# Kernel optimization log

Measured on AMD Instinct MI355X. Metric: run time of the kernel, lower is better.

The kernel has to match this reference:

```python
import jax, jax.numpy as jnp
import numpy as np

B, C = 8, 2048          # batch, out_dim (projection channels)
HG = WG = 32            # global crop feature map
HL = WL = 12            # local crop feature map
STUDENT_TEMP = 0.1
TEMP_SCHEDULE = np.concatenate([np.linspace(0.04, 0.07, 30), np.ones(100 - 30) * 0.07])

# Fixed relative boxes (x1, x2, y1, y2) per (iq, v) crop pair, shared across the
# batch so grid shapes are static. Source computes grid_H from teacher_feat.shape[0]
# (= C, a quirk of the original code) and grid_W from shape[1] (= spatial H); boxes
# are chosen so resulting grids are ~[22-25, 22-24].
PAIRS = [
    (0, 1, (-0.80, 0.70, -0.500, -0.475), (-0.90, 0.60, -0.60, 0.60)),
    (0, 2, (-0.75, 0.75,  0.100,  0.125), (-0.80, 0.80, -0.80, 0.80)),
    (0, 3, (-0.60, 0.90, -0.200, -0.178), (-0.70, 0.90, -0.90, 0.70)),
    (1, 0, (-0.70, 0.80,  0.300,  0.322), (-0.85, 0.65, -0.50, 0.90)),
    (1, 2, (-0.90, 0.50, -0.100, -0.076), (-0.60, 0.95, -0.95, 0.60)),
    (1, 3, (-0.50, 0.95,  0.200,  0.224), (-0.90, 0.90, -0.40, 0.95)),
]


def _grid_dims(box, Hc, Wc):
    x1, x2, y1, y2 = box
    return int(abs(y1 - y2) / 2 * Hc), int(abs(x1 - x2) / 2 * Wc)  # (grid_H, grid_W)


def _make_grid(box, gH, gW):
    # Faithful to source: meshgrid([linspace(y1,y2,gH), linspace(x1,x2,gW)]),
    # stacked so channel 0 holds the y-linspace (which grid_sample reads as x).
    x1, x2, y1, y2 = box
    yy, xx = jnp.meshgrid(jnp.linspace(y1, y2, gH), jnp.linspace(x1, x2, gW), indexing='ij')
    return jnp.stack([yy, xx], axis=-1)  # [gH, gW, 2]


def _grid_sample_border(img, grid):
    # torch.nn.functional.grid_sample, bilinear, padding_mode='border',
    # align_corners=False. img: [B, C, H, W], grid: [gH, gW, 2] (same grid per batch).
    H, W = img.shape[-2], img.shape[-1]
    gx, gy = grid[..., 0], grid[..., 1]
    ix = jnp.clip((gx + 1.0) * (W * 0.5) - 0.5, 0.0, W - 1.0)  # border: clip coords
    iy = jnp.clip((gy + 1.0) * (H * 0.5) - 0.5, 0.0, H - 1.0)
    x0f, y0f = jnp.floor(ix), jnp.floor(iy)
    wx = (ix - x0f)[None, None]  # [1,1,gH,gW]
    wy = (iy - y0f)[None, None]
    x0 = x0f.astype(jnp.int32)
    y0 = y0f.astype(jnp.int32)
    x1 = jnp.minimum(x0 + 1, W - 1)
    y1 = jnp.minimum(y0 + 1, H - 1)
    v00 = img[:, :, y0, x0]
    v01 = img[:, :, y0, x1]
    v10 = img[:, :, y1, x0]
    v11 = img[:, :, y1, x1]
    return (1.0 - wy) * ((1.0 - wx) * v00 + wx * v01) + wy * ((1.0 - wx) * v10 + wx * v11)


def setup_inputs() -> dict:
    key = jax.random.key(0)
    ks = jax.random.split(key, 7)
    return {
        'student_g0': jax.random.normal(ks[0], (B, C, HG, WG), jnp.float32),
        'student_g1': jax.random.normal(ks[1], (B, C, HG, WG), jnp.float32),
        'student_l0': jax.random.normal(ks[2], (B, C, HL, WL), jnp.float32),
        'student_l1': jax.random.normal(ks[3], (B, C, HL, WL), jnp.float32),
        'teacher_g0': jax.random.normal(ks[4], (B, C, HG, WG), jnp.float32),
        'teacher_g1': jax.random.normal(ks[5], (B, C, HG, WG), jnp.float32),
        'center': jax.random.normal(ks[6], (1, C), jnp.float32) * 0.1,
        'epoch': 5,
    }


def reference(student_g0, student_g1, student_l0, student_l1,
              teacher_g0, teacher_g1, center, epoch):
    temp = float(TEMP_SCHEDULE[epoch])
    students = [s / STUDENT_TEMP for s in (student_g0, student_g1, student_l0, student_l1)]
    cen = center[:, :, None, None]  # [1,C,1,1]
    cteach = [jax.nn.softmax((t - cen) / temp, axis=1) for t in (teacher_g0, teacher_g1)]

    losses = []
    for iq, v, tbox, sbox in PAIRS:
        tfeat = cteach[iq]   # [B,C,H,W]
        sfeat = students[v]  # [B,C,h,w]
        # Faithful: source passes (shape[0]=C, shape[1]=spatial H) as (H, W).
        gH, gW = _grid_dims(tbox, C, tfeat.shape[2])
        t_common = jax.lax.stop_gradient(_grid_sample_border(tfeat, _make_grid(tbox, gH, gW)))
        s_common = _grid_sample_border(sfeat, _make_grid(sbox, gH, gW))
        # cross-entropy over channels -> [B, gH, gW]
        loss = (-t_common * jax.nn.log_softmax(s_common, axis=1)).sum(axis=1)
        losses.append(loss.reshape(-1))
    return jnp.concatenate(losses).mean()
```

## Files before the change

### kernel.cpp

```cpp
#include <hip/hip_runtime.h>
#include <hip/hip_fp16.h>

#define NPOS 26688

struct PairInfo {
  int iq, v, Hs, gH, gW, base, per;
  unsigned magicPer, magicW;
  int tOfs, tN, tCb;
  int sN, sCb;
  float tx1, tx2, ty1, ty2;
  float sx1, sx2, sy1, sy2;
};

__constant__ PairInfo g_pairs[6] = {
  {0,1,32,25,24,    0,600, 7158279u,178956971u,    0,2, 7, 22,5, -0.80f,0.70f,-0.500f,-0.475f,  -0.90f,0.60f,-0.60f,0.60f},
  {0,2,12,25,24, 4800,600, 7158279u,178956971u,  512,2,17, 12,0, -0.75f,0.75f, 0.100f, 0.125f,  -0.80f,0.80f,-0.80f,0.80f},
  {0,3,12,22,24, 9600,528, 8134408u,178956971u, 1024,2,12, 12,0, -0.60f,0.90f,-0.200f,-0.178f,  -0.70f,0.90f,-0.90f,0.70f},
  {1,0,32,22,24,13824,528, 8134408u,178956971u, 1536,2,20, 24,7, -0.70f,0.80f, 0.300f, 0.322f,  -0.85f,0.65f,-0.50f,0.90f},
  {1,2,12,24,22,18048,528, 8134408u,195225787u, 2048,3,13, 12,0, -0.90f,0.50f,-0.100f,-0.076f,  -0.60f,0.95f,-0.95f,0.60f},
  {1,3,12,24,23,22272,552, 7780739u,186737709u, 2816,3,18, 12,0, -0.50f,0.95f, 0.200f, 0.224f,  -0.90f,0.90f,-0.40f,0.95f},
};

__constant__ int g_tentX[2][8] = {
  { 7, 8,12,13,17,18,-100,-100},
  {13,14,15,18,19,20,  20,  21},
};
__constant__ int g_tentO[2][8] = {
  {   0,   0,1024,1024, 512, 512,   0,   0},
  {2048,2048,2048,2816,2816,2816,1536,1536},
};
__constant__ int g_tentN[2][8] = {
  {2,2,2,2,2,2,2,2},
  {3,3,3,3,3,3,2,2},
};
__constant__ int g_tentC[2][8] = {
  {0,1,0,1,0,1,0,0},
  {0,1,2,0,1,2,0,1},
};
__constant__ int g_cumTex[6] = {0, 512, 1024, 1536, 2048, 2816};
__constant__ int g_tN[6]    = {2, 2, 2, 2, 3, 3};
__constant__ int g_tCb[6]   = {7, 17, 12, 20, 13, 18};

__device__ inline float get_invtemp(const int* __restrict__ ep) {
  int e = ep[0];
  e = e < 0 ? 0 : (e > 99 ? 99 : e);
  float temp = (e < 30) ? (0.04f + (float)e * (0.03f / 29.0f)) : 0.07f;
  return 1.0f / temp;
}

__device__ inline float sel4(const float4& v, int q) {
  return q == 0 ? v.x : q == 1 ? v.y : q == 2 ? v.z : v.w;
}

typedef _Float16 hv2 __attribute__((ext_vector_type(2)));
__device__ inline float fdot2f(__half2 a, __half2 b, float c) {
#if defined(__has_builtin)
#if __has_builtin(__builtin_amdgcn_fdot2)
  return __builtin_amdgcn_fdot2(*reinterpret_cast<hv2*>(&a),
                                *reinterpret_cast<hv2*>(&b), c, false);
#else
  float2 af = __half22float2(a), bf = __half22float2(b);
  return fmaf(af.x, bf.x, fmaf(af.y, bf.y, c));
#endif
#else
  float2 af = __half22float2(a), bf = __half22float2(b);
  return fmaf(af.x, bf.x, fmaf(af.y, bf.y, c));
#endif
}

__global__ __launch_bounds__(256) void dino_phase1(
    const float* __restrict__ tg0, const float* __restrict__ tg1,
    const float* __restrict__ cen, const int* __restrict__ ep,
    float* __restrict__ part_m, float* __restrict__ part_s,
    __half* __restrict__ Tc,
    const float* __restrict__ sl0, const float* __restrict__ sl1,
    __half* __restrict__ Sl0, __half* __restrict__ Sl1,
    const float* __restrict__ sg0, const float* __restrict__ sg1,
    __half* __restrict__ Sg0, __half* __restrict__ Sg1) {
  __shared__ float smem[2960];
  int bid = blockIdx.x;
  int t = threadIdx.x;

  if (bid < 4096) {
    int chunk = bid & 7;
    int y = (bid >> 3) & 31;
    int b = (bid >> 8) & 7;
    int view = bid >> 11;
    const float* __restrict__ src = view ? tg1 : tg0;
    float invtemp = get_invtemp(ep);

    float* cenl = smem;
    float* pm   = smem + 256;
    float* ps   = smem + 1312;
    float* pm2  = smem + 2368;
    float* ps2  = smem + 2632;
    float* cm   = smem + 2896;

    cenl[t] = cen[chunk * 256 + t];
    __syncthreads();

    int xg = t & 7, sub = t >> 3;
    const float* sp = src + (((size_t)(b * 2048 + chunk * 256 + sub)) * 32 + y) * 32 + xg * 4;
    float4 lg[8];
#pragma unroll
    for (int k = 0; k < 8; ++k) {
      float4 v = *reinterpret_cast<const float4*>(sp + (size_t)k * 32768);
      float cv = cenl[k * 32 + sub];
      lg[k].x = (v.x - cv) * invtemp;
      lg[k].y = (v.y - cv) * invtemp;
      lg[k].z = (v.z - cv) * invtemp;
      lg[k].w = (v.w - cv) * invtemp;
    }
    float4 mx = lg[0];
#pragma unroll
    for (int k = 1; k < 8; ++k) {
      mx.x = fmaxf(mx.x, lg[k].x); mx.y = fmaxf(mx.y, lg[k].y);
      mx.z = fmaxf(mx.z, lg[k].z); mx.w = fmaxf(mx.w, lg[k].w);
    }
    float4 s = make_float4(0.f, 0.f, 0.f, 0.f);
#pragma unroll
    for (int k = 0; k < 8; ++k) {
      s.x += __expf(lg[k].x - mx.x); s.y += __expf(lg[k].y - mx.y);
      s.z += __expf(lg[k].z - mx.z); s.w += __expf(lg[k].w - mx.w);
    }
    pm[sub * 33 + xg * 4 + 0] = mx.x; ps[sub * 33 + xg * 4 + 0] = s.x;
    pm[sub * 33 + xg * 4 + 1] = mx.y; ps[sub * 33 + xg * 4 + 1] = s.y;
    pm[sub * 33 + xg * 4 + 2] = mx.z; ps[sub * 33 + xg * 4 + 2] = s.z;
    pm[sub * 33 + xg * 4 + 3] = mx.w; ps[sub * 33 + xg * 4 + 3] = s.w;
    __syncthreads();
    {
      int x = t & 31, g = t >> 5;
      float m0 = pm[(g * 4 + 0) * 33 + x], m1 = pm[(g * 4 + 1) * 33 + x];
      float m2 = pm[(g * 4 + 2) * 33 + x], m3 = pm[(g * 4 + 3) * 33 + x];
      float M = fmaxf(fmaxf(m0, m1), fmaxf(m2, m3));
      float S = ps[(g * 4 + 0) * 33 + x] * __expf(m0 - M)
              + ps[(g * 4 + 1) * 33 + x] * __expf(m1 - M)
              + ps[(g * 4 + 2) * 33 + x] * __expf(m2 - M)
              + ps[(g * 4 + 3) * 33 + x] * __expf(m3 - M);
      pm2[g * 33 + x] = M; ps2[g * 33 + x] = S;
    }
    __syncthreads();
    if (t < 32) {
      float M = pm2[t];
#pragma unroll
      for (int g = 1; g < 8; ++g) M = fmaxf(M, pm2[g * 33 + t]);
      float S = 0.f;
#pragma unroll
      for (int g = 0; g < 8; ++g) S += ps2[g * 33 + t] * __expf(pm2[g * 33 + t] - M);
      part_m[bid * 32 + t] = M;
      part_s[bid * 32 + t] = S;
      cm[t] = M;
    }
    __syncthreads();
    int nent = view ? 8 : 6;
#pragma unroll
    for (int e = 0; e < 8; ++e) {
      if (e < nent) {
        int ex = g_tentX[view][e];
        if ((ex >> 2) == xg) {
          int q = ex & 3;
          float cmx = cm[ex & 31];
          int tex = g_tentO[view][e] + (b * 32 + y) * g_tentN[view][e] + g_tentC[view][e];
          tex = min(max(tex, 0), 3583);
          size_t base = (size_t)tex * 2048 + chunk * 256 + sub;
#pragma unroll
          for (int k = 0; k < 8; ++k)
            Tc[base + k * 32] = __float2half(sel4(lg[k], q) - cmx);
        }
      }
    }
    return;
  }

  if (bid < 6144) {
    float* tile = smem;
    int lb = bid - 4096;
    int ct = lb & 127;
    int g = lb >> 7;
    int b = g & 7;
    int vv = g >> 3;
    const float* __restrict__ src = vv ? sl1 : sl0;
    __half* __restrict__ dst = vv ? Sl1 : Sl0;
    const float* sp = src + ((size_t)(b * 2048 + ct * 16)) * 144;
#pragma unroll
    for (int k = 0; k < 9; ++k) {
      int idx = t + 256 * k;
      int c = idx / 144;
      int yx = idx - c * 144;
      tile[c * 145 + yx] = sp[idx] * 10.f;
    }
    __syncthreads();
    __half* dp = dst + ((size_t)(b * 144)) * 2048 + ct * 16;
#pragma unroll
    for (int k = 0; k < 2; ++k) {
      int u = t + 256 * k;
      if (u < 288) {
        int yx = u >> 1, q8 = (u & 1) * 8;
        __half hv[8];
#pragma unroll
        for (int j = 0; j < 8; ++j) hv[j] = __float2half(tile[(q8 + j) * 145 + yx]);
        *reinterpret_cast<float4*>(dp + (size_t)yx * 2048 + q8) =
            *reinterpret_cast<float4*>(hv);
      }
    }
    return;
  }

  float* tile = smem;
  int lb = bid - 6144;
  int ct = lb & 31;
  int t2 = lb >> 5;
  int yi = t2 % 26;
  int g = t2 / 26;
  int y = yi + 1;
  int b = g & 7;
  int which = g >> 3;
  const float* __restrict__ src = which ? sg1 : sg0;
  __half* __restrict__ dst = which ? Sg1 : Sg0;
  int cb = which ? 5 : 7;
  int n = which ? 22 : 24;

  int xg = t & 7, ch = t >> 3;
  const float* sp = src + (((size_t)(b * 2048 + ct * 64 + ch)) * 32 + y) * 32 + xg * 4;
  float4 v0 = *reinterpret_cast<const float4*>(sp);
  float4 v1 = *reinterpret_cast<const float4*>(sp + 32768);
  tile[ch * 33 + xg * 4 + 0] = v0.x * 10.f;
  tile[ch * 33 + xg * 4 + 1] = v0.y * 10.f;
  tile[ch * 33 + xg * 4 + 2] = v0.z * 10.f;
  tile[ch * 33 + xg * 4 + 3] = v0.w * 10.f;
  tile[(ch + 32) * 33 + xg * 4 + 0] = v1.x * 10.f;
  tile[(ch + 32) * 33 + xg * 4 + 1] = v1.y * 10.f;
  tile[(ch + 32) * 33 + xg * 4 + 2] = v1.z * 10.f;
  tile[(ch + 32) * 33 + xg * 4 + 3] = v1.w * 10.f;
  __syncthreads();
  int xx = t >> 3, ccq = (t & 7) * 8;
  if (xx >= cb && xx < cb + n) {
    __half hv[8];
#pragma unroll
    for (int j = 0; j < 8; ++j) hv[j] = __float2half(tile[(ccq + j) * 33 + xx]);
    __half* dp = dst + ((size_t)((b * 32 + y) * n + (xx - cb))) * 2048 + ct * 64 + ccq;
    *reinterpret_cast<float4*>(dp) = *reinterpret_cast<float4*>(hv);
  }
}

union H8 { uint4 u; __half2 h[4]; };

__global__ __launch_bounds__(256) void dino_probs(
    const __half* __restrict__ Tc, __half* __restrict__ Tp,
    const float* __restrict__ part_m, const float* __restrict__ part_s) {
  __shared__ float pm8[8], ps8[8];
  int bid = blockIdx.x;
  int t = threadIdx.x;
  int p = 0;
#pragma unroll
  for (int q = 1; q < 6; ++q) p += (bid >= g_cumTex[q]) ? 1 : 0;
  int r = bid - g_cumTex[p];
  int n = g_tN[p];
  int by = (n == 2) ? (r >> 1) : (r / 3);
  by = min(max(by, 0), 255);
  int ci = min(max(r - by * n, 0), n - 1);
  int x = g_tCb[p] + ci;
  int view = (p >= 3) ? 1 : 0;
  int b = by >> 5, y = by & 31;
  int texRow = ((view * 8 + b) * 32 + y);
  if (t < 8) {
    pm8[t] = part_m[(texRow * 8 + t) * 32 + x];
    ps8[t] = part_s[(texRow * 8 + t) * 32 + x];
  }
  __syncthreads();
  float M = pm8[0];
#pragma unroll
  for (int c = 1; c < 8; ++c) M = fmaxf(M, pm8[c]);
  float S = 0.f;
#pragma unroll
  for (int c = 0; c < 8; ++c) S += ps8[c] * __expf(pm8[c] - M);
  float invS = 1.f / S;
  float off = pm8[t >> 5] - M;

  int tex = min(g_cumTex[p] + by * n + ci, 3583);
  size_t base = (size_t)tex * 2048 + t * 8;
  H8 hh;
  hh.u = *reinterpret_cast<const uint4*>(Tc + base);
#pragma unroll
  for (int pc = 0; pc < 4; ++pc) {
    float2 f = __half22float2(hh.h[pc]);
    f.x = __expf(f.x + off) * invS;
    f.y = __expf(f.y + off) * invS;
    hh.h[pc] = __floats2half2_rn(f.x, f.y);
  }
  *reinterpret_cast<uint4*>(Tp + base) = hh.u;
}

__global__ __launch_bounds__(256) void dino_main(
    const __half* __restrict__ Tp,
    const __half* __restrict__ S0, const __half* __restrict__ S1,
    const __half* __restrict__ S2, const __half* __restrict__ S3,
    float* __restrict__ losses) {
  int wid = threadIdx.x >> 6, lane = threadIdx.x & 63;
  int pair = blockIdx.x / 1200;
  int slot = blockIdx.x - pair * 1200;
  PairInfo pi = g_pairs[pair];
  int posInPair = slot * 4 + wid;
  if (posInPair >= pi.per * 8) return;

  unsigned up = (unsigned)posInPair;
  int b = (int)__umulhi(up, pi.magicPer);
  b = min(max(b, 0), 7);
  int r = posInPair - b * pi.per;
  r = min(max(r, 0), pi.per - 1);
  int i = (int)__umulhi((unsigned)r, pi.magicW);
  i = min(max(i, 0), pi.gH - 1);
  int j = r - i * pi.gW;
  j = min(max(j, 0), pi.gW - 1);

  float tyy = pi.ty1 + (float)i * (pi.ty2 - pi.ty1) / (float)(pi.gH - 1);
  float txx = pi.tx1 + (float)j * (pi.tx2 - pi.tx1) / (float)(pi.gW - 1);
  float tix = fminf(fmaxf((tyy + 1.0f) * 16.0f - 0.5f, 0.0f), 31.0f);
  float tiy = fminf(fmaxf((txx + 1.0f) * 16.0f - 0.5f, 0.0f), 31.0f);
  int tx0 = (int)tix, ty0 = (int)tiy;
  float wxt = tix - (float)tx0, wyt = tiy - (float)ty0;
  int tx1i = min(tx0 + 1, 31), ty1i = min(ty0 + 1, 31);

  int hs = pi.Hs;
  float hh = 0.5f * (float)hs, hm = (float)(hs - 1);
  float syy = pi.sy1 + (float)i * (pi.sy2 - pi.sy1) / (float)(pi.gH - 1);
  float sxx = pi.sx1 + (float)j * (pi.sx2 - pi.sx1) / (float)(pi.gW - 1);
  float six = fminf(fmaxf((syy + 1.0f) * hh - 0.5f, 0.0f), hm);
  float siy = fminf(fmaxf((sxx + 1.0f) * hh - 0.5f, 0.0f), hm);
  int sx0 = (int)six, sy0 = (int)siy;
  float wxs = six - (float)sx0, wys = siy - (float)sy0;
  int sx1i = min(sx0 + 1, hs - 1), sy1i = min(sy0 + 1, hs - 1);

  const __half* __restrict__ S =
      (pi.v == 0) ? S0 : (pi.v == 1) ? S1 : (pi.v == 2) ? S2 : S3;

  int tc0 = min(max(tx0 - pi.tCb, 0), pi.tN - 1);
  int tc1 = min(max(tx1i - pi.tCb, 0), pi.tN - 1);
  int trow = pi.tOfs + (b * 32 + ty0) * pi.tN;
  int trow1 = pi.tOfs + (b * 32 + ty1i) * pi.tN;
  int toff00 = min(trow + tc0, 3583) * 2048;
  int toff01 = min(trow + tc1, 3583) * 2048;
  int toff10 = min(trow1 + tc0, 3583) * 2048;
  int toff11 = min(trow1 + tc1, 3583) * 2048;
  int sc0 = min(max(sx0 - pi.sCb, 0), pi.sN - 1);
  int sc1 = min(max(sx1i - pi.sCb, 0), pi.sN - 1);
  int soff00 = ((b * hs + sy0) * pi.sN + sc0) * 2048;
  int soff01 = ((b * hs + sy0) * pi.sN + sc1) * 2048;
  int soff10 = ((b * hs + sy1i) * pi.sN + sc0) * 2048;
  int soff11 = ((b * hs + sy1i) * pi.sN + sc1) * 2048;

  __half2 wt00 = __float2half2_rn((1.f - wyt) * (1.f - wxt));
  __half2 wt01 = __float2half2_rn((1.f - wyt) * wxt);
  __half2 wt10 = __float2half2_rn(wyt * (1.f - wxt));
  __half2 wt11 = __float2half2_rn(wyt * wxt);
  __half2 ws00 = __float2half2_rn((1.f - wys) * (1.f - wxs));
  __half2 ws01 = __float2half2_rn((1.f - wys) * wxs);
  __half2 ws10 = __float2half2_rn(wys * (1.f - wxs));
  __half2 ws11 = __float2half2_rn(wys * wxs);

  float sum = 0.f, dot = 0.f;
#pragma unroll
  for (int k = 0; k < 4; ++k) {
    int c0 = (k << 9) + (lane << 3);
    H8 t00, t01, t10, t11, a00, a01, a10, a11;
    t00.u = *reinterpret_cast<const uint4*>(Tp + toff00 + c0);
    t01.u = *reinterpret_cast<const uint4*>(Tp + toff01 + c0);
    t10.u = *reinterpret_cast<const uint4*>(Tp + toff10 + c0);
    t11.u = *reinterpret_cast<const uint4*>(Tp + toff11 + c0);
    a00.u = *reinterpret_cast<const uint4*>(S + soff00 + c0);
    a01.u = *reinterpret_cast<const uint4*>(S + soff01 + c0);
    a10.u = *reinterpret_cast<const uint4*>(S + soff10 + c0);
    a11.u = *reinterpret_cast<const uint4*>(S + soff11 + c0);
#pragma unroll
    for (int p = 0; p < 4; ++p) {
      __half2 tc2 = __hmul2(wt00, t00.h[p]);
      tc2 = __hfma2(wt01, t01.h[p], tc2);
      tc2 = __hfma2(wt10, t10.h[p], tc2);
      tc2 = __hfma2(wt11, t11.h[p], tc2);
      __half2 sc2 = __hmul2(ws00, a00.h[p]);
      sc2 = __hfma2(ws01, a01.h[p], sc2);
      sc2 = __hfma2(ws10, a10.h[p], sc2);
      sc2 = __hfma2(ws11, a11.h[p], sc2);
      dot = fdot2f(tc2, sc2, dot);
      float2 scf = __half22float2(sc2);
      sum += __expf(scf.x);
      sum += __expf(scf.y);
    }
  }
#pragma unroll
  for (int off = 32; off; off >>= 1) {
    sum += __shfl_down(sum, off);
    dot += __shfl_down(dot, off);
  }
  if (lane == 0) losses[pi.base + posInPair] = logf(sum) - dot;
}

__global__ __launch_bounds__(1024) void dino_reduce(const float* __restrict__ losses,
                                                    float* __restrict__ out) {
  __shared__ double sd[1024];
  int t = threadIdx.x;
  double a = 0.0;
  for (int i4 = t; i4 < 6672; i4 += 1024) {
    float4 v = *reinterpret_cast<const float4*>(losses + i4 * 4);
    a += (double)v.x + (double)v.y + (double)v.z + (double)v.w;
  }
  sd[t] = a;
  __syncthreads();
  for (int off = 512; off; off >>= 1) {
    if (t < off) sd[t] += sd[t + off];
    __syncthreads();
  }
  if (t == 0) out[0] = (float)(sd[0] / (double)NPOS);
}

extern "C" void kernel_launch(void* const* d_in, const int* in_sizes, int n_in,
                              void* d_out, int out_size, void* d_ws, size_t ws_size,
                              hipStream_t stream) {
  const float* sg0 = (const float*)d_in[0];
  const float* sg1 = (const float*)d_in[1];
  const float* sl0 = (const float*)d_in[2];
  const float* sl1 = (const float*)d_in[3];
  const float* tg0 = (const float*)d_in[4];
  const float* tg1 = (const float*)d_in[5];
  const float* cen = (const float*)d_in[6];
  const int* epoch = (const int*)d_in[7];
  float* out = (float*)d_out;
  char* w = (char*)d_ws;

  const size_t OFF_LOSS= 131072;
  const size_t OFF_PM  = 262144;
  const size_t OFF_PS  = 1310720;
  const size_t OFF_TC  = 2359296;
  const size_t OFF_TP  = 17039360;
  const size_t OFF_SG0 = 31719424;
  const size_t OFF_SG1 = 56885248;
  const size_t OFF_SL0 = 79953920;
  const size_t OFF_SL1 = 84672512;

  float* losses = (float*)(w + OFF_LOSS);
  float* part_m = (float*)(w + OFF_PM);
  float* part_s = (float*)(w + OFF_PS);
  __half* Tc  = (__half*)(w + OFF_TC);
  __half* Tp  = (__half*)(w + OFF_TP);
  __half* Sg0 = (__half*)(w + OFF_SG0);
  __half* Sg1 = (__half*)(w + OFF_SG1);
  __half* Sl0 = (__half*)(w + OFF_SL0);
  __half* Sl1 = (__half*)(w + OFF_SL1);

  dino_phase1<<<19456, 256, 0, stream>>>(tg0, tg1, cen, epoch, part_m, part_s, Tc,
                                         sl0, sl1, Sl0, Sl1, sg0, sg1, Sg0, Sg1);
  dino_probs<<<3584, 256, 0, stream>>>(Tc, Tp, part_m, part_s);
  dino_main<<<7200, 256, 0, stream>>>(Tp, Sg0, Sg1, Sl0, Sl1, losses);
  dino_reduce<<<1, 1024, 0, stream>>>(losses, out);
}
```

Baseline: 114.0 us.

## Restructure teacher softmax stats pass to per-block channel groups with online softmax

The teacher pre-pass now gives each block a 32-channel group across the full 32x32 spatial plane, instead of 256 channels of one row. Each thread keeps an online max/sum and writes the partials straight out, which removes the multi-stage shared-memory reductions and barriers. Logits for the needed x columns are staged in shared memory so each thread can emit a contiguous 32-half slice of Tc with vector stores. The probs kernel now merges 64 partials per position with a wavefront shuffle reduction instead of 8. The cost is a larger partials buffer, more shared memory per block, and fewer teacher blocks.

```diff
diff --git a/kernel.cpp b/kernel.cpp
--- a/kernel.cpp
+++ b/kernel.cpp
@@ -21,6 +21,10 @@
   {1,3,12,24,23,22272,552, 7780739u,186737709u, 2816,3,18, 12,0, -0.50f,0.95f, 0.200f, 0.224f,  -0.90f,0.90f,-0.40f,0.95f},
 };
 
+__constant__ int g_ux[2][32] = {
+  {-1,-1,-1,-1,-1,-1,-1, 0, 1,-1,-1,-1, 2, 3,-1,-1,-1, 4, 5,-1,-1,-1,-1,-1,-1,-1,-1,-1,-1,-1,-1,-1},
+  {-1,-1,-1,-1,-1,-1,-1,-1,-1,-1,-1,-1,-1, 0, 1, 2,-1,-1, 3, 4, 5, 6,-1,-1,-1,-1,-1,-1,-1,-1,-1,-1},
+};
 __constant__ int g_tentX[2][8] = {
   { 7, 8,12,13,17,18,-100,-100},
   {13,14,15,18,19,20,  20,  21},
@@ -77,104 +81,73 @@
     __half* __restrict__ Sl0, __half* __restrict__ Sl1,
     const float* __restrict__ sg0, const float* __restrict__ sg1,
     __half* __restrict__ Sg0, __half* __restrict__ Sg1) {
-  __shared__ float smem[2960];
+  __shared__ float smem[7424];
   int bid = blockIdx.x;
   int t = threadIdx.x;
 
-  if (bid < 4096) {
-    int chunk = bid & 7;
-    int y = (bid >> 3) & 31;
-    int b = (bid >> 8) & 7;
-    int view = bid >> 11;
+  if (bid < 1024) {
+    int cg = bid & 63;
+    int b = (bid >> 6) & 7;
+    int view = bid >> 9;
     const float* __restrict__ src = view ? tg1 : tg0;
     float invtemp = get_invtemp(ep);
-
-    float* cenl = smem;
-    float* pm   = smem + 256;
-    float* ps   = smem + 1312;
-    float* pm2  = smem + 2368;
-    float* ps2  = smem + 2632;
-    float* cm   = smem + 2896;
-
-    cenl[t] = cen[chunk * 256 + t];
+    float* cenl = smem + 7392;
+    if (t < 32) cenl[t] = cen[cg * 32 + t];
     __syncthreads();
 
-    int xg = t & 7, sub = t >> 3;
-    const float* sp = src + (((size_t)(b * 2048 + chunk * 256 + sub)) * 32 + y) * 32 + xg * 4;
-    float4 lg[8];
-#pragma unroll
-    for (int k = 0; k < 8; ++k) {
-      float4 v = *reinterpret_cast<const float4*>(sp + (size_t)k * 32768);
-      float cv = cenl[k * 32 + sub];
-      lg[k].x = (v.x - cv) * invtemp;
-      lg[k].y = (v.y - cv) * invtemp;
-      lg[k].z = (v.z - cv) * invtemp;
-      lg[k].w = (v.w - cv) * invtemp;
+    int y = t >> 3, x0 = (t & 7) * 4;
+    int y33 = y * 33;
+    int s0 = g_ux[view][x0], s1 = g_ux[view][x0 + 1];
+    int s2 = g_ux[view][x0 + 2], s3 = g_ux[view][x0 + 3];
+    const float* base = src + ((size_t)(b * 2048 + cg * 32)) * 1024 + t * 4;
+
+    float4 m4 = make_float4(-1e30f, -1e30f, -1e30f, -1e30f);
+    float4 s4 = make_float4(0.f, 0.f, 0.f, 0.f);
+#pragma unroll 4
+    for (int c = 0; c < 32; ++c) {
+      float4 v = *reinterpret_cast<const float4*>(base + (size_t)c * 1024);
+      float cv = cenl[c];
+      float4 lg;
+      lg.x = (v.x - cv) * invtemp; lg.y = (v.y - cv) * invtemp;
+      lg.z = (v.z - cv) * invtemp; lg.w = (v.w - cv) * invtemp;
+      if (s0 >= 0) smem[s0 * 1056 + y33 + c] = lg.x;
+      if (s1 >= 0) smem[s1 * 1056 + y33 + c] = lg.y;
+      if (s2 >= 0) smem[s2 * 1056 + y33 + c] = lg.z;
+      if (s3 >= 0) smem[s3 * 1056 + y33 + c] = lg.w;
+      float mn;
+      mn = fmaxf(m4.x, lg.x); s4.x = s4.x * __expf(m4.x - mn) + __expf(lg.x - mn); m4.x = mn;
+      mn = fmaxf(m4.y, lg.y); s4.y = s4.y * __expf(m4.y - mn) + __expf(lg.y - mn); m4.y = mn;
+      mn = fmaxf(m4.z, lg.z); s4.z = s4.z * __expf(m4.z - mn) + __expf(lg.z - mn); m4.z = mn;
+      mn = fmaxf(m4.w, lg.w); s4.w = s4.w * __expf(m4.w - mn) + __expf(lg.w - mn); m4.w = mn;
     }
-    float4 mx = lg[0];
-#pragma unroll
-    for (int k = 1; k < 8; ++k) {
-      mx.x = fmaxf(mx.x, lg[k].x); mx.y = fmaxf(mx.y, lg[k].y);
-      mx.z = fmaxf(mx.z, lg[k].z); mx.w = fmaxf(mx.w, lg[k].w);
-    }
-    float4 s = make_float4(0.f, 0.f, 0.f, 0.f);
-#pragma unroll
-    for (int k = 0; k < 8; ++k) {
-      s.x += __expf(lg[k].x - mx.x); s.y += __expf(lg[k].y - mx.y);
-      s.z += __expf(lg[k].z - mx.z); s.w += __expf(lg[k].w - mx.w);
-    }
-    pm[sub * 33 + xg * 4 + 0] = mx.x; ps[sub * 33 + xg * 4 + 0] = s.x;
-    pm[sub * 33 + xg * 4 + 1] = mx.y; ps[sub * 33 + xg * 4 + 1] = s.y;
-    pm[sub * 33 + xg * 4 + 2] = mx.z; ps[sub * 33 + xg * 4 + 2] = s.z;
-    pm[sub * 33 + xg * 4 + 3] = mx.w; ps[sub * 33 + xg * 4 + 3] = s.w;
-    __syncthreads();
-    {
-      int x = t & 31, g = t >> 5;
-      float m0 = pm[(g * 4 + 0) * 33 + x], m1 = pm[(g * 4 + 1) * 33 + x];
-      float m2 = pm[(g * 4 + 2) * 33 + x], m3 = pm[(g * 4 + 3) * 33 + x];
-      float M = fmaxf(fmaxf(m0, m1), fmaxf(m2, m3));
-      float S = ps[(g * 4 + 0) * 33 + x] * __expf(m0 - M)
-              + ps[(g * 4 + 1) * 33 + x] * __expf(m1 - M)
-              + ps[(g * 4 + 2) * 33 + x] * __expf(m2 - M)
-              + ps[(g * 4 + 3) * 33 + x] * __expf(m3 - M);
-      pm2[g * 33 + x] = M; ps2[g * 33 + x] = S;
-    }
-    __syncthreads();
-    if (t < 32) {
-      float M = pm2[t];
-#pragma unroll
-      for (int g = 1; g < 8; ++g) M = fmaxf(M, pm2[g * 33 + t]);
-      float S = 0.f;
-#pragma unroll
-      for (int g = 0; g < 8; ++g) S += ps2[g * 33 + t] * __expf(pm2[g * 33 + t] - M);
-      part_m[bid * 32 + t] = M;
-      part_s[bid * 32 + t] = S;
-      cm[t] = M;
-    }
-    __syncthreads();
-    int nent = view ? 8 : 6;
+    size_t prow = ((size_t)((view * 8 + b) * 64 + cg)) * 1024 + t * 4;
+    *reinterpret_cast<float4*>(part_m + prow) = m4;
+    *reinterpret_cast<float4*>(part_s + prow) = s4;
+
 #pragma unroll
     for (int e = 0; e < 8; ++e) {
-      if (e < nent) {
-        int ex = g_tentX[view][e];
-        if ((ex >> 2) == xg) {
-          int q = ex & 3;
-          float cmx = cm[ex & 31];
-          int tex = g_tentO[view][e] + (b * 32 + y) * g_tentN[view][e] + g_tentC[view][e];
-          tex = min(max(tex, 0), 3583);
-          size_t base = (size_t)tex * 2048 + chunk * 256 + sub;
-#pragma unroll
-          for (int k = 0; k < 8; ++k)
-            Tc[base + k * 32] = __float2half(sel4(lg[k], q) - cmx);
-        }
+      int ex = g_tentX[view][e];
+      int d = ex - x0;
+      if (d >= 0 && d < 4) {
+        int slot = g_ux[view][ex];
+        float mm = sel4(m4, d);
+        int tex = g_tentO[view][e] + (b * 32 + y) * g_tentN[view][e] + g_tentC[view][e];
+        tex = min(max(tex, 0), 3583);
+        __half hv[32];
+#pragma unroll
+        for (int c = 0; c < 32; ++c)
+          hv[c] = __float2half(smem[slot * 1056 + y33 + c] - mm);
+        uint4* dst = reinterpret_cast<uint4*>(Tc + (size_t)tex * 2048 + cg * 32);
+        const uint4* sv = reinterpret_cast<const uint4*>(hv);
+        dst[0] = sv[0]; dst[1] = sv[1]; dst[2] = sv[2]; dst[3] = sv[3];
       }
     }
     return;
   }
 
-  if (bid < 6144) {
+  if (bid < 3072) {
     float* tile = smem;
-    int lb = bid - 4096;
+    int lb = bid - 1024;
     int ct = lb & 127;
     int g = lb >> 7;
     int b = g & 7;
@@ -207,7 +180,7 @@
   }
 
   float* tile = smem;
-  int lb = bid - 6144;
+  int lb = bid - 3072;
   int ct = lb & 31;
   int t2 = lb >> 5;
   int yi = t2 % 26;
@@ -248,7 +221,7 @@
 __global__ __launch_bounds__(256) void dino_probs(
     const __half* __restrict__ Tc, __half* __restrict__ Tp,
     const float* __restrict__ part_m, const float* __restrict__ part_s) {
-  __shared__ float pm8[8], ps8[8];
+  __shared__ float pr[66];
   int bid = blockIdx.x;
   int t = threadIdx.x;
   int p = 0;
@@ -262,20 +235,23 @@
   int x = g_tCb[p] + ci;
   int view = (p >= 3) ? 1 : 0;
   int b = by >> 5, y = by & 31;
-  int texRow = ((view * 8 + b) * 32 + y);
-  if (t < 8) {
-    pm8[t] = part_m[(texRow * 8 + t) * 32 + x];
-    ps8[t] = part_s[(texRow * 8 + t) * 32 + x];
+  int vb = view * 8 + b;
+
+  if (t < 64) {
+    float mg = part_m[((size_t)(vb * 64 + t)) * 1024 + y * 32 + x];
+    float sg = part_s[((size_t)(vb * 64 + t)) * 1024 + y * 32 + x];
+    pr[t] = mg;
+    float M = mg;
+#pragma unroll
+    for (int off = 32; off; off >>= 1) M = fmaxf(M, __shfl_xor(M, off));
+    float sv = sg * __expf(mg - M);
+#pragma unroll
+    for (int off = 32; off; off >>= 1) sv += __shfl_xor(sv, off);
+    if (t == 0) { pr[64] = M; pr[65] = 1.f / sv; }
   }
   __syncthreads();
-  float M = pm8[0];
-#pragma unroll
-  for (int c = 1; c < 8; ++c) M = fmaxf(M, pm8[c]);
-  float S = 0.f;
-#pragma unroll
-  for (int c = 0; c < 8; ++c) S += ps8[c] * __expf(pm8[c] - M);
-  float invS = 1.f / S;
-  float off = pm8[t >> 5] - M;
+  float off = pr[t >> 2] - pr[64];
+  float invS = pr[65];
 
   int tex = min(g_cumTex[p] + by * n + ci, 3583);
   size_t base = (size_t)tex * 2048 + t * 8;
@@ -429,13 +405,13 @@
 
   const size_t OFF_LOSS= 131072;
   const size_t OFF_PM  = 262144;
-  const size_t OFF_PS  = 1310720;
-  const size_t OFF_TC  = 2359296;
-  const size_t OFF_TP  = 17039360;
-  const size_t OFF_SG0 = 31719424;
-  const size_t OFF_SG1 = 56885248;
-  const size_t OFF_SL0 = 79953920;
-  const size_t OFF_SL1 = 84672512;
+  const size_t OFF_PS  = 4456448;
+  const size_t OFF_TC  = 8650752;
+  const size_t OFF_TP  = 23330816;
+  const size_t OFF_SG0 = 38010880;
+  const size_t OFF_SG1 = 63176704;
+  const size_t OFF_SL0 = 86245376;
+  const size_t OFF_SL1 = 90963968;
 
   float* losses = (float*)(w + OFF_LOSS);
   float* part_m = (float*)(w + OFF_PM);
@@ -447,7 +423,7 @@
   __half* Sl0 = (__half*)(w + OFF_SL0);
   __half* Sl1 = (__half*)(w + OFF_SL1);
 
-  dino_phase1<<<19456, 256, 0, stream>>>(tg0, tg1, cen, epoch, part_m, part_s, Tc,
+  dino_phase1<<<16384, 256, 0, stream>>>(tg0, tg1, cen, epoch, part_m, part_s, Tc,
                                          sl0, sl1, Sl0, Sl1, sg0, sg1, Sg0, Sg1);
   dino_probs<<<3584, 256, 0, stream>>>(Tc, Tp, part_m, part_s);
   dino_main<<<7200, 256, 0, stream>>>(Tp, Sg0, Sg1, Sl0, Sl1, losses);
```

Result: slower. 122.6 us (+7.5%).
